# Kernel tuning notes

Measured on AMD Instinct MI355X. Metric: run time of the kernel, lower is better.

The kernel has to match this reference:

```python
import jax, jax.numpy as jnp
import numpy as np
from jax import lax

# ---- configuration (matches init_kwargs) ----
B, C_DATA, C_FEAT, H, W = 2, 8, 8, 160, 160
K = 7                      # number of soft nearest neighbors
PS, STRIDE, WIN = 10, 5, 15
FEAT, C_EMB = 64, 8
N1 = (H - PS) // STRIDE + 1   # 31, no padding needed
N2 = (W - PS) // STRIDE + 1   # 31
NEG_INF = -1e9


def _conv3(x, w, b):
    y = lax.conv_general_dilated(x, w, (1, 1), 'SAME',
                                 dimension_numbers=('NCHW', 'OIHW', 'NCHW'))
    return y + b[None, :, None, None]


def _cnn(x, w1, b1, w2, b2, w3, b3):
    # depth-3 DnCNN-style net: conv-relu-conv-relu-conv (bn=False, lastact=linear)
    h = jax.nn.relu(_conv3(x, w1, b1))
    h = jax.nn.relu(_conv3(h, w2, b2))
    return _conv3(h, w3, b3)


def _im2patch(x):
    # x: [b,c,H,W] -> [b,n1,n2,c*PS*PS]; patch flattened channel-major (c,p1,p2)
    ii = jnp.arange(N1)[:, None] * STRIDE + jnp.arange(PS)[None, :]  # [n1,PS]
    jj = jnp.arange(N2)[:, None] * STRIDE + jnp.arange(PS)[None, :]  # [n2,PS]
    p = x[:, :, ii[:, None, :, None], jj[None, :, None, :]]  # [b,c,n1,n2,PS,PS]
    p = jnp.transpose(p, (0, 2, 3, 1, 4, 5))
    return p.reshape(p.shape[0], N1, N2, -1)


def _n3block(x_data, x_faet, ew1, eb1, ew2, eb2, ew3, eb3,
             tw1, tb1, tw2, tb2, tw3, tb3):
    xe = _cnn(x_faet, ew1, eb1, ew2, eb2, ew3, eb3)      # [b,8,H,W] embeddings
    log_temp = _cnn(x_faet, tw1, tb1, tw2, tb2, tw3, tb3)  # [b,1,H,W]

    ye = _im2patch(xe)                        # [b,n1,n2,E]; queries == database
    yp = _im2patch(x_data)                    # [b,n1,n2,F]
    lt = _im2patch(log_temp).mean(-1)         # scalar log-temp per patch
    temp = jnp.exp(lt)[..., None]             # [b,n1,n2,1] (temp_bias = 1)

    S = min(WIN, N1, N2)
    R = S // 2
    base1 = jnp.clip(jnp.arange(N1) - R, 0, N1 - S)   # clamped window top-left
    base2 = jnp.clip(jnp.arange(N2) - R, 0, N2 - S)
    offs = jnp.stack(jnp.meshgrid(jnp.arange(S), jnp.arange(S), indexing='ij'),
                     axis=-1).reshape(-1, 2)          # [S*S,2]
    i1, i2 = jnp.arange(N1), jnp.arange(N2)
    yn = jnp.sum(ye * ye, axis=-1)            # [b,n1,n2] squared norms

    @jax.checkpoint
    def dist_step(carry, off):
        j1 = base1 + off[0]
        j2 = base2 + off[1]
        xs = ye[:, j1][:, :, j2]              # [b,n1,n2,E] candidate embedding
        xn = yn[:, j1][:, :, j2]
        dot = jnp.einsum('bije,bije->bij', ye, xs)
        d = yn + xn - 2.0 * dot               # squared euclidean distance
        self_m = (j1 == i1)[:, None] & (j2 == i2)[None, :]
        return carry, (d, self_m)

    _, (D, selfm) = lax.scan(dist_step, None, offs)
    D = jnp.moveaxis(D, 0, -1)                # [b,n1,n2,O], O=S*S
    selfm = jnp.moveaxis(selfm, 0, -1)        # [n1,n2,O]

    logits = -D / temp
    logits = jnp.where(selfm, NEG_INF, logits)   # exclude_self

    # continuous deterministic top-k (N3Net): w_j = softmax(a); a += log(1 - w_j)
    ws = []
    for _ in range(K):
        wgt = jax.nn.softmax(logits, axis=-1)
        ws.append(wgt)
        logits = logits + jnp.log1p(-jnp.minimum(wgt, 1.0 - 1e-6))
    Wk = jnp.stack(ws, axis=-1)               # [b,n1,n2,O,K]

    @jax.checkpoint
    def agg_step(z, args):
        off, wk = args                        # wk: [b,n1,n2,K]
        j1 = base1 + off[0]
        j2 = base2 + off[1]
        ys = yp[:, j1][:, :, j2]              # [b,n1,n2,F]
        return z + wk[..., :, None] * ys[..., None, :], None

    z0 = jnp.zeros(yp.shape[:3] + (K, yp.shape[-1]), yp.dtype)
    z, _ = lax.scan(agg_step, z0, (offs, jnp.moveaxis(Wk, 3, 0)))
    z = z - yp[..., None, :]                  # residue=True
    out_p = jnp.concatenate([yp[..., None, :], z], axis=3)  # [b,n1,n2,K+1,F]

    # fold patch volumes back to image, averaging overlaps
    b = out_p.shape[0]
    C = (K + 1) * C_DATA
    out_p = out_p.reshape(b, N1, N2, K + 1, C_DATA, PS, PS)
    out_p = jnp.transpose(out_p, (0, 3, 4, 1, 2, 5, 6)).reshape(b, C, N1, N2, PS, PS)
    rows = jnp.arange(N1)[:, None] * STRIDE + jnp.arange(PS)[None, :]
    cols = jnp.arange(N2)[:, None] * STRIDE + jnp.arange(PS)[None, :]
    lin = (rows[:, None, :, None] * W + cols[None, :, None, :]).reshape(-1)
    vals = out_p.reshape(b, C, -1)
    img = jnp.zeros((b, C, H * W), out_p.dtype).at[:, :, lin].add(vals)
    cnt = jnp.zeros((H * W,), out_p.dtype).at[lin].add(1.0)
    return (img / cnt).reshape(b, C, H, W)


def setup_inputs() -> dict:
    key = jax.random.key(0)
    ks = jax.random.split(key, 8)
    f32 = jnp.float32
    wn = lambda k, s: jax.random.normal(k, s, f32) * 0.05
    return dict(
        x_data=jax.random.normal(ks[0], (B, C_DATA, H, W), f32),
        x_faet=jax.random.normal(ks[1], (B, C_FEAT, H, W), f32),
        ew1=wn(ks[2], (FEAT, C_FEAT, 3, 3)), eb1=jnp.zeros((FEAT,), f32),
        ew2=wn(ks[3], (FEAT, FEAT, 3, 3)), eb2=jnp.zeros((FEAT,), f32),
        ew3=wn(ks[4], (C_EMB, FEAT, 3, 3)), eb3=jnp.zeros((C_EMB,), f32),
        tw1=wn(ks[5], (FEAT, C_FEAT, 3, 3)), tb1=jnp.zeros((FEAT,), f32),
        tw2=wn(ks[6], (FEAT, FEAT, 3, 3)), tb2=jnp.zeros((FEAT,), f32),
        tw3=wn(ks[7], (1, FEAT, 3, 3)), tb3=jnp.zeros((1,), f32),
    )


def reference(x_data, x_faet, ew1, eb1, ew2, eb2, ew3, eb3,
              tw1, tb1, tw2, tb2, tw3, tb3):
    return _n3block(x_data, x_faet, ew1, eb1, ew2, eb2, ew3, eb3,
                    tw1, tb1, tw2, tb2, tw3, tb3)
```

## Files before the change

kernel.cpp:

```cpp
#include <hip/hip_runtime.h>
#include <math.h>

#define BN 2
#define HH 160
#define WW 160
#define CDATA 8
#define PS 10
#define STR 5
#define N1 31
#define N2 31
#define NSITE (N1*N2)
#define SITES (BN*NSITE)
#define SWIN 15
#define NOFF 225
#define KK 7
#define EDIM 800
#define NPIX 25600
#define LP 40
#define KP 480
#define COLP 992
#define GP 34
#define KSPLIT 5

typedef __attribute__((ext_vector_type(8))) short s8v;
typedef __attribute__((ext_vector_type(8))) unsigned short u8v;
typedef __attribute__((ext_vector_type(4))) unsigned short u4v;
typedef __attribute__((ext_vector_type(4))) float f4v;

__device__ __forceinline__ unsigned short f2bf(float f) {
    unsigned u = __float_as_uint(f);
    return (unsigned short)((u + 0x7FFFu + ((u >> 16) & 1u)) >> 16);
}
__device__ __forceinline__ float bf2f(unsigned short h) {
    return __uint_as_float(((unsigned)h) << 16);
}

__global__ __launch_bounds__(256) void prep_k(const float* __restrict__ xd,
                                              const float* __restrict__ ew2,
                                              const float* __restrict__ tw2,
                                              const float* __restrict__ ew1,
                                              const float* __restrict__ tw1,
                                              const float* __restrict__ ew3,
                                              const float* __restrict__ tw3,
                                              unsigned short* __restrict__ ypT,
                                              unsigned short* __restrict__ wp,
                                              unsigned short* __restrict__ wp1,
                                              unsigned short* __restrict__ wp3) {
    int blk = blockIdx.x;
    int t = threadIdx.x;
    if (blk < 1600) {
        int b = blk / 800, e = blk % 800;
        int cd = e & 7, pp = e >> 3;
        int pi = pp / 10, pj = pp % 10;
        const float* src = xd + ((size_t)(b * 8 + cd) * HH + pi) * WW + pj;
        unsigned short* dst = ypT + (size_t)blk * COLP;
        for (int it = 0; it < 4; ++it) {
            int col = it * 256 + t;
            if (col < COLP) {
                int j1 = col >> 5, j2 = col & 31;
                unsigned short v = 0;
                if (j2 < 31) v = f2bf(src[(j1 * 5) * WW + j2 * 5]);
                dst[col] = v;
            }
        }
    } else if (blk < 1888) {
        int idx = (blk - 1600) * 256 + t;
        int which = idx / (64 * 576); int r = idx % (64 * 576);
        int n = r / 576, k = r % 576;
        int p = k / 64, c = k % 64;
        const float* w = which ? tw2 : ew2;
        wp[idx] = f2bf(w[(n * 64 + c) * 9 + p]);
    } else if (blk < 1936) {
        int idx = (blk - 1888) * 256 + t;
        if (idx < 128 * 96) {
            int n = idx / 96, k = idx % 96;
            int tap = k >> 3, c = k & 7;
            unsigned short v = 0;
            if (tap < 9) {
                const float* w = (n < 64) ? ew1 : tw1;
                v = f2bf(w[((n & 63) * 8 + c) * 9 + tap]);
            }
            wp1[idx] = v;
        }
    } else {
        int idx = (blk - 1936) * 256 + t;
        if (idx < 2 * 16 * 576) {
            int which = idx / (16 * 576); int r = idx % (16 * 576);
            int n = r / 576, k = r % 576;
            int tap = k / 64, c = k % 64;
            float w = 0.f; bool lo = false;
            if (which == 0) { w = ew3[((n & 7) * 64 + c) * 9 + tap]; lo = (n >= 8); }
            else if (n < 2) { w = tw3[c * 9 + tap]; lo = (n == 1); }
            unsigned short hi = f2bf(w);
            wp3[idx] = lo ? f2bf(w - bf2f(hi)) : hi;
            if (which == 1 && n >= 2) wp3[idx] = 0;
        }
    }
}

__global__ __launch_bounds__(256) void conv1_mfma_k(const float* __restrict__ xf,
                                                    const unsigned short* __restrict__ wp1,
                                                    const float* __restrict__ eb1,
                                                    const float* __restrict__ tb1,
                                                    unsigned short* __restrict__ h1) {
    __shared__ unsigned short Al[128 * LP];
    __shared__ unsigned short Bl[64 * LP];
    const int t = threadIdx.x;
    const int m0 = blockIdx.x * 64;
    const int wv = t >> 6, lane = t & 63;
    f4v acc[2][4];
    #pragma unroll
    for (int fj = 0; fj < 2; ++fj)
        #pragma unroll
        for (int fi = 0; fi < 4; ++fi) { f4v z = {0.f,0.f,0.f,0.f}; acc[fj][fi] = z; }
    const int mp = m0 + (t >> 2);
    const int b = mp / NPIX, rp = mp % NPIX;
    const int py = rp / WW, px = rp % WW;
    for (int ks = 0; ks < 3; ++ks) {
        int tap = ks * 4 + (t & 3);
        int dy = tap / 3 - 1, dx = tap % 3 - 1;
        int yy = py + dy, xx = px + dx;
        bool ok = (tap < 9) && yy >= 0 && yy < HH && xx >= 0 && xx < WW;
        u8v bv;
        #pragma unroll
        for (int c = 0; c < 8; ++c)
            bv[c] = ok ? f2bf(xf[((size_t)(b * 8 + c)) * NPIX + yy * WW + xx]) : 0;
        __syncthreads();
        *(u8v*)(Bl + (t >> 2) * LP + (t & 3) * 8) = bv;
        #pragma unroll
        for (int it = 0; it < 2; ++it) {
            int idx = t + it * 256;
            int row = idx >> 2, seg = idx & 3;
            *(u8v*)(Al + row * LP + seg * 8) = *(const u8v*)(wp1 + row * 96 + ks * 32 + seg * 8);
        }
        __syncthreads();
        s8v af[2], bf[4];
        #pragma unroll
        for (int fj = 0; fj < 2; ++fj)
            af[fj] = *(const s8v*)((const short*)Al + (wv * 32 + fj * 16 + (lane & 15)) * LP + (lane >> 4) * 8);
        #pragma unroll
        for (int fi = 0; fi < 4; ++fi)
            bf[fi] = *(const s8v*)((const short*)Bl + (fi * 16 + (lane & 15)) * LP + (lane >> 4) * 8);
        #pragma unroll
        for (int fj = 0; fj < 2; ++fj)
            #pragma unroll
            for (int fi = 0; fi < 4; ++fi)
                acc[fj][fi] = __builtin_amdgcn_mfma_f32_16x16x32_bf16(af[fj], bf[fi], acc[fj][fi], 0, 0, 0);
    }
    #pragma unroll
    for (int fj = 0; fj < 2; ++fj) {
        int nb = wv * 32 + fj * 16 + (lane >> 4) * 4;
        float bias4[4];
        #pragma unroll
        for (int c = 0; c < 4; ++c) {
            int n = nb + c;
            bias4[c] = (n < 64) ? eb1[n] : tb1[n - 64];
        }
        #pragma unroll
        for (int fi = 0; fi < 4; ++fi) {
            int mm = m0 + fi * 16 + (lane & 15);
            ushort4 o;
            o.x = f2bf(fmaxf(acc[fj][fi][0] + bias4[0], 0.f));
            o.y = f2bf(fmaxf(acc[fj][fi][1] + bias4[1], 0.f));
            o.z = f2bf(fmaxf(acc[fj][fi][2] + bias4[2], 0.f));
            o.w = f2bf(fmaxf(acc[fj][fi][3] + bias4[3], 0.f));
            *(ushort4*)(h1 + (size_t)mm * 128 + nb) = o;
        }
    }
}

__global__ __launch_bounds__(256) void conv2_mfma_k(const unsigned short* __restrict__ h1,
                                                    const unsigned short* __restrict__ wp,
                                                    const float* __restrict__ eb2,
                                                    const float* __restrict__ tb2,
                                                    unsigned short* __restrict__ h2) {
    __shared__ unsigned short Al[64 * LP];
    __shared__ unsigned short Bl[128 * LP];
    const int t = threadIdx.x;
    const int which = blockIdx.y;
    const int m0 = blockIdx.x * 128;
    const int wv = t >> 6, lane = t & 63;
    f4v acc[4][2];
    #pragma unroll
    for (int nf = 0; nf < 4; ++nf)
        #pragma unroll
        for (int mf = 0; mf < 2; ++mf) { f4v z = {0.f,0.f,0.f,0.f}; acc[nf][mf] = z; }
    const unsigned short* wb = wp + (size_t)which * 64 * 576;
    const int sm = t >> 2, sq = (t & 3) * 8;
    const int mp0 = m0 + sm;
    const int b0 = mp0 / NPIX, rp0 = mp0 % NPIX;
    const int py0 = rp0 / WW, px0 = rp0 % WW;
    const int mp1 = m0 + 64 + sm;
    const int b1_ = mp1 / NPIX, rp1 = mp1 % NPIX;
    const int py1 = rp1 / WW, px1 = rp1 % WW;
    for (int step = 0; step < 18; ++step) {
        const int p = step >> 1, ch = (step & 1) * 32;
        const int dy = p / 3 - 1, dx = p % 3 - 1;
        s8v av = *(const s8v*)(wb + sm * 576 + p * 64 + ch + sq);
        s8v bv0, bv1;
        #pragma unroll
        for (int j = 0; j < 8; j++) { bv0[j] = 0; bv1[j] = 0; }
        int yy = py0 + dy, xx = px0 + dx;
        if (yy >= 0 && yy < HH && xx >= 0 && xx < WW)
            bv0 = *(const s8v*)((const short*)h1 + ((size_t)b0 * NPIX + yy * WW + xx) * 128 + which * 64 + ch + sq);
        yy = py1 + dy; xx = px1 + dx;
        if (yy >= 0 && yy < HH && xx >= 0 && xx < WW)
            bv1 = *(const s8v*)((const short*)h1 + ((size_t)b1_ * NPIX + yy * WW + xx) * 128 + which * 64 + ch + sq);
        __syncthreads();
        *(s8v*)((short*)Al + sm * LP + sq) = av;
        *(s8v*)((short*)Bl + sm * LP + sq) = bv0;
        *(s8v*)((short*)Bl + (64 + sm) * LP + sq) = bv1;
        __syncthreads();
        s8v af[4], bf[2];
        #pragma unroll
        for (int nf = 0; nf < 4; ++nf)
            af[nf] = *(const s8v*)((const short*)Al + (nf * 16 + (lane & 15)) * LP + (lane >> 4) * 8);
        #pragma unroll
        for (int mf = 0; mf < 2; ++mf)
            bf[mf] = *(const s8v*)((const short*)Bl + (wv * 32 + mf * 16 + (lane & 15)) * LP + (lane >> 4) * 8);
        #pragma unroll
        for (int nf = 0; nf < 4; ++nf)
            #pragma unroll
            for (int mf = 0; mf < 2; ++mf)
                acc[nf][mf] = __builtin_amdgcn_mfma_f32_16x16x32_bf16(af[nf], bf[mf], acc[nf][mf], 0, 0, 0);
    }
    const float* bias = which ? tb2 : eb2;
    #pragma unroll
    for (int nf = 0; nf < 4; ++nf) {
        int nb = nf * 16 + (lane >> 4) * 4;
        f4v bv4 = *(const f4v*)(bias + nb);
        #pragma unroll
        for (int mf = 0; mf < 2; ++mf) {
            int mm = m0 + wv * 32 + mf * 16 + (lane & 15);
            ushort4 o;
            o.x = f2bf(fmaxf(acc[nf][mf][0] + bv4[0], 0.f));
            o.y = f2bf(fmaxf(acc[nf][mf][1] + bv4[1], 0.f));
            o.z = f2bf(fmaxf(acc[nf][mf][2] + bv4[2], 0.f));
            o.w = f2bf(fmaxf(acc[nf][mf][3] + bv4[3], 0.f));
            *(ushort4*)(h2 + ((size_t)which * 51200 + mm) * 64 + nb) = o;
        }
    }
}

__global__ __launch_bounds__(256) void conv3_mfma_k(const unsigned short* __restrict__ h2,
                                                    const unsigned short* __restrict__ wp3,
                                                    const float* __restrict__ eb3,
                                                    const float* __restrict__ tb3,
                                                    unsigned short* __restrict__ xeH,
                                                    unsigned short* __restrict__ xeL,
                                                    float* __restrict__ splane,
                                                    float* __restrict__ ltm) {
    __shared__ unsigned short Al[16 * LP];
    __shared__ unsigned short Bl[128 * LP];
    const int t = threadIdx.x;
    const int which = blockIdx.y;
    const int m0 = blockIdx.x * 128;
    const int wv = t >> 6, lane = t & 63;
    f4v acc[2];
    { f4v z = {0.f,0.f,0.f,0.f}; acc[0] = z; acc[1] = z; }
    const unsigned short* wb = wp3 + (size_t)which * 16 * 576;
    const int sm = t >> 2, sq = (t & 3) * 8;
    const int mp0 = m0 + sm;
    const int b0 = mp0 / NPIX, rp0 = mp0 % NPIX;
    const int py0 = rp0 / WW, px0 = rp0 % WW;
    const int mp1 = m0 + 64 + sm;
    const int b1_ = mp1 / NPIX, rp1 = mp1 % NPIX;
    const int py1 = rp1 / WW, px1 = rp1 % WW;
    for (int step = 0; step < 18; ++step) {
        const int p = step >> 1, ch = (step & 1) * 32;
        const int dy = p / 3 - 1, dx = p % 3 - 1;
        s8v av;
        if (t < 64) av = *(const s8v*)(wb + (t >> 2) * 576 + p * 64 + ch + (t & 3) * 8);
        s8v bv0, bv1;
        #pragma unroll
        for (int j = 0; j < 8; j++) { bv0[j] = 0; bv1[j] = 0; }
        int yy = py0 + dy, xx = px0 + dx;
        if (yy >= 0 && yy < HH && xx >= 0 && xx < WW)
            bv0 = *(const s8v*)((const short*)h2 + ((size_t)which * 51200 + (size_t)b0 * NPIX + yy * WW + xx) * 64 + ch + sq);
        yy = py1 + dy; xx = px1 + dx;
        if (yy >= 0 && yy < HH && xx >= 0 && xx < WW)
            bv1 = *(const s8v*)((const short*)h2 + ((size_t)which * 51200 + (size_t)b1_ * NPIX + yy * WW + xx) * 64 + ch + sq);
        __syncthreads();
        if (t < 64) *(s8v*)((short*)Al + (t >> 2) * LP + (t & 3) * 8) = av;
        *(s8v*)((short*)Bl + sm * LP + sq) = bv0;
        *(s8v*)((short*)Bl + (64 + sm) * LP + sq) = bv1;
        __syncthreads();
        s8v af = *(const s8v*)((const short*)Al + (lane & 15) * LP + (lane >> 4) * 8);
        #pragma unroll
        for (int mf = 0; mf < 2; ++mf) {
            s8v bf = *(const s8v*)((const short*)Bl + (wv * 32 + mf * 16 + (lane & 15)) * LP + (lane >> 4) * 8);
            acc[mf] = __builtin_amdgcn_mfma_f32_16x16x32_bf16(af, bf, acc[mf], 0, 0, 0);
        }
    }
    #pragma unroll
    for (int mf = 0; mf < 2; ++mf) {
        int mm = m0 + wv * 32 + mf * 16 + (lane & 15);
        if (which == 0) {
            f4v hilo;
            #pragma unroll
            for (int c = 0; c < 4; ++c)
                hilo[c] = acc[mf][c] + __shfl_xor(acc[mf][c], 32);
            if (lane < 32) {
                int nb = (lane >> 4) * 4;
                u4v hs, ls;
                float ss = 0.f;
                #pragma unroll
                for (int c = 0; c < 4; ++c) {
                    float v = hilo[c] + eb3[nb + c];
                    unsigned short h = f2bf(v);
                    hs[c] = h;
                    ls[c] = f2bf(v - bf2f(h));
                    ss += v * v;
                }
                *(u4v*)(xeH + (size_t)mm * 8 + nb) = hs;
                *(u4v*)(xeL + (size_t)mm * 8 + nb) = ls;
                ss += __shfl_xor(ss, 16);
                if (lane < 16) splane[mm] = ss;
            }
        } else {
            if ((lane >> 4) == 0)
                ltm[mm] = acc[mf][0] + acc[mf][1] + tb3[0];
        }
    }
}

__global__ __launch_bounds__(256) void ynt_k(const float* __restrict__ splane,
                                             const float* __restrict__ ltm,
                                             float* __restrict__ yn,
                                             float* __restrict__ tempv) {
    int wv = threadIdx.x >> 6, lane = threadIdx.x & 63;
    int wid = blockIdx.x * 4 + wv;
    if (wid >= SITES) return;
    int b = wid / NSITE; int ij = wid % NSITE;
    int i1 = ij / N2, i2 = ij % N2;
    float s1 = 0.f, s2 = 0.f;
    for (int p = lane; p < 100; p += 64) {
        int rr = p / 10, q = p % 10;
        int idx = b * NPIX + (i1 * STR + rr) * WW + i2 * STR + q;
        s1 += splane[idx];
        s2 += ltm[idx];
    }
    #pragma unroll
    for (int o = 32; o; o >>= 1) { s1 += __shfl_xor(s1, o); s2 += __shfl_xor(s2, o); }
    if (lane == 0) {
        yn[wid] = s1;
        tempv[wid] = expf(s2 * (1.f / 100.f));
    }
}

__global__ __launch_bounds__(256) void gram_mfma_k(const unsigned short* __restrict__ xeH,
                                                   const unsigned short* __restrict__ xeL,
                                                   float* __restrict__ dotsC) {
    __shared__ unsigned short AsH[32 * GP], AsL[32 * GP];
    __shared__ unsigned short BsH[256 * GP], BsL[256 * GP];
    int blk = blockIdx.x;
    int kc = blk % KSPLIT; int r = blk / KSPLIT;
    int nh = r & 1; r >>= 1;
    int b = r / N1, i1 = r % N1;
    int b1 = min(max(i1 - 7, 0), 16);
    int t = threadIdx.x;
    int wv = t >> 6, lane = t & 63;
    f4v acc[2][4];
    #pragma unroll
    for (int mt = 0; mt < 2; ++mt)
        #pragma unroll
        for (int nt = 0; nt < 4; ++nt) { f4v z = {0.f,0.f,0.f,0.f}; acc[mt][nt] = z; }
    const size_t pbase = (size_t)b * NPIX;
    for (int ks = kc * 5; ks < kc * 5 + 5; ++ks) {
        __syncthreads();
        {
            int idx = t & 127;
            int row = idx >> 2, seg = idx & 3;
            int p = ks * 4 + seg;
            int rr = p / 10, q = p - rr * 10;
            u8v v;
            #pragma unroll
            for (int u = 0; u < 8; ++u) v[u] = 0;
            if (row < 31) {
                size_t a = (pbase + (size_t)(i1 * STR + rr) * WW + row * STR + q) * 8;
                v = *(const u8v*)((t < 128 ? xeH : xeL) + a);
            }
            *(u8v*)((t < 128 ? AsH : AsL) + row * GP + seg * 8) = v;
        }
        #pragma unroll
        for (int rep = 0; rep < 8; ++rep) {
            int idx = t + rep * 256;
            int isH = idx < 1024;
            int id2 = idx & 1023;
            int row = id2 >> 2, seg = id2 & 3;
            int dj = nh * 8 + (row >> 5), j2 = row & 31;
            int p = ks * 4 + seg;
            int rr = p / 10, q = p - rr * 10;
            u8v v;
            #pragma unroll
            for (int u = 0; u < 8; ++u) v[u] = 0;
            if (dj < 15 && j2 < 31) {
                size_t a = (pbase + (size_t)((b1 + dj) * STR + rr) * WW + j2 * STR + q) * 8;
                v = *(const u8v*)((isH ? xeH : xeL) + a);
            }
            *(u8v*)((isH ? BsH : BsL) + row * GP + seg * 8) = v;
        }
        __syncthreads();
        s8v afH[2], afL[2], bfH[4], bfL[4];
        #pragma unroll
        for (int mt = 0; mt < 2; ++mt) {
            int ar = mt * 16 + (lane & 15);
            afH[mt] = *(const s8v*)((const short*)AsH + ar * GP + (lane >> 4) * 8);
            afL[mt] = *(const s8v*)((const short*)AsL + ar * GP + (lane >> 4) * 8);
        }
        #pragma unroll
        for (int nt = 0; nt < 4; ++nt) {
            int br = wv * 64 + nt * 16 + (lane & 15);
            bfH[nt] = *(const s8v*)((const short*)BsH + br * GP + (lane >> 4) * 8);
            bfL[nt] = *(const s8v*)((const short*)BsL + br * GP + (lane >> 4) * 8);
        }
        #pragma unroll
        for (int mt = 0; mt < 2; ++mt)
            #pragma unroll
            for (int nt = 0; nt < 4; ++nt) {
                acc[mt][nt] = __builtin_amdgcn_mfma_f32_16x16x32_bf16(afH[mt], bfH[nt], acc[mt][nt], 0, 0, 0);
                acc[mt][nt] = __builtin_amdgcn_mfma_f32_16x16x32_bf16(afH[mt], bfL[nt], acc[mt][nt], 0, 0, 0);
                acc[mt][nt] = __builtin_amdgcn_mfma_f32_16x16x32_bf16(afL[mt], bfH[nt], acc[mt][nt], 0, 0, 0);
            }
    }
    float* dk = dotsC + (size_t)kc * SITES * NOFF;
    #pragma unroll
    for (int mt = 0; mt < 2; ++mt) {
        int i2b = mt * 16 + (lane >> 4) * 4;
        #pragma unroll
        for (int nt = 0; nt < 4; ++nt) {
            int n = wv * 64 + nt * 16 + (lane & 15);
            int dj = nh * 8 + (n >> 5), j2 = n & 31;
            if (dj >= 15 || j2 >= 31) continue;
            #pragma unroll
            for (int c = 0; c < 4; ++c) {
                int i2 = i2b + c;
                if (i2 >= 31) continue;
                int b2 = min(max(i2 - 7, 0), 16);
                int dc = j2 - b2;
                if (dc < 0 || dc >= SWIN) continue;
                size_t site = (size_t)((b * N1 + i1) * N2 + i2);
                dk[site * NOFF + dj * SWIN + dc] = acc[mt][nt][c];
            }
        }
    }
}

__global__ __launch_bounds__(256) void softmax_awrite_k(const float* __restrict__ dotsC,
                                                        const float* __restrict__ yn,
                                                        const float* __restrict__ tempv,
                                                        unsigned short* __restrict__ Aglob) {
    __shared__ float sw[4][228];
    int wv = threadIdx.x >> 6, lane = threadIdx.x & 63;
    int wid = blockIdx.x * 4 + wv;
    bool active = (wid < SITES);
    int wids = active ? wid : (SITES - 1);
    int b = wids / NSITE; int ij = wids % NSITE;
    int i1 = ij / N2, i2 = ij % N2;
    int b1 = min(max(i1 - 7, 0), 16);
    int b2 = min(max(i2 - 7, 0), 16);
    int pglob = i2 >> 1, s = i2 & 1;
    unsigned short* Abase = Aglob + (size_t)((b * N1 + i1) * 256) * KP;
    float yns = yn[wids];
    float tvi = 1.f / tempv[wids];
    float lg[4];
    #pragma unroll
    for (int r = 0; r < 4; ++r) {
        int t = lane + 64 * r;
        lg[r] = -1e9f;
        if (t < NOFF) {
            float dot = 0.f;
            #pragma unroll
            for (int kc = 0; kc < KSPLIT; ++kc)
                dot += dotsC[((size_t)kc * SITES + wids) * NOFF + t];
            int dj = t / SWIN, dc = t % SWIN;
            int j1 = b1 + dj, j2 = b2 + dc;
            float xn = yn[(b * N1 + j1) * N2 + j2];
            float d = yns + xn - 2.f * dot;
            lg[r] = -d * tvi;
            if (j1 == i1 && j2 == i2) lg[r] = -1e9f;
        }
    }
    for (int k = 0; k < KK; ++k) {
        float m = fmaxf(fmaxf(lg[0], lg[1]), fmaxf(lg[2], lg[3]));
        #pragma unroll
        for (int o = 32; o; o >>= 1) m = fmaxf(m, __shfl_xor(m, o));
        float ex[4]; float ssum = 0.f;
        #pragma unroll
        for (int r = 0; r < 4; ++r) { ex[r] = __expf(lg[r] - m); ssum += ex[r]; }
        #pragma unroll
        for (int o = 32; o; o >>= 1) ssum += __shfl_xor(ssum, o);
        float inv = 1.f / ssum;
        #pragma unroll
        for (int r = 0; r < 4; ++r) {
            float wgt = ex[r] * inv;
            int t = lane + 64 * r;
            if (t < NOFF) sw[wv][t] = wgt;
            lg[r] += log1pf(-fminf(wgt, 1.f - 1e-6f));
        }
        __syncthreads();
        if (active && lane < 60) {
            u8v o;
            #pragma unroll
            for (int u = 0; u < 8; ++u) {
                int n = lane * 8 + u;
                int dj = n >> 5, j2 = n & 31;
                int dc = j2 - b2;
                o[u] = (j2 < 31 && dc >= 0 && dc < SWIN) ? f2bf(sw[wv][dj * SWIN + dc]) : (unsigned short)0;
            }
            int m_ = 16 * pglob + k + 7 * s;
            *(u8v*)(Abase + (size_t)m_ * KP + lane * 8) = o;
        }
        __syncthreads();
    }
    if (active && s == 0 && lane < 60) {
        u8v z;
        #pragma unroll
        for (int u = 0; u < 8; ++u) z[u] = 0;
        *(u8v*)(Abase + (size_t)(16 * pglob + 14) * KP + lane * 8) = z;
        *(u8v*)(Abase + (size_t)(16 * pglob + 15) * KP + lane * 8) = z;
        if (i2 == 30) {
            #pragma unroll
            for (int sl = 7; sl < 14; ++sl)
                *(u8v*)(Abase + (size_t)(16 * 15 + sl) * KP + lane * 8) = z;
        }
    }
}

__global__ __launch_bounds__(256) void agg_gemm_k(const unsigned short* __restrict__ Aglob,
                                                  const unsigned short* __restrict__ ypT,
                                                  unsigned short* __restrict__ zbuf) {
    __shared__ unsigned short As[128 * 40];
    __shared__ unsigned short Bs[160 * 40];
    int blk = blockIdx.x;
    int b = blk / 310; int r = blk % 310;
    int i1 = r / 10; int r2 = r % 10;
    int mh = r2 / 5, nc = r2 % 5;
    int b1 = min(max(i1 - 7, 0), 16);
    int t = threadIdx.x;
    int wv = t >> 6, lane = t & 63;
    int wm = (wv & 1) * 64, we = (wv >> 1) * 80;
    const unsigned short* Ab = Aglob + ((size_t)(b * N1 + i1) * 256 + mh * 128) * KP;
    const unsigned short* Bb = ypT + ((size_t)b * 800 + nc * 160) * COLP + b1 * 32;
    f4v accr[4][5];
    #pragma unroll
    for (int mt = 0; mt < 4; ++mt)
        #pragma unroll
        for (int et = 0; et < 5; ++et) { f4v z = {0.f,0.f,0.f,0.f}; accr[mt][et] = z; }
    for (int ks = 0; ks < 15; ++ks) {
        __syncthreads();
        #pragma unroll
        for (int it = 0; it < 2; ++it) {
            int idx = t + it * 256;
            int row = idx >> 2, seg = idx & 3;
            *(u8v*)(As + row * 40 + seg * 8) = *(const u8v*)(Ab + (size_t)row * KP + ks * 32 + seg * 8);
        }
        #pragma unroll
        for (int it = 0; it < 3; ++it) {
            int idx = t + it * 256;
            if (idx < 640) {
                int row = idx >> 2, seg = idx & 3;
                *(u8v*)(Bs + row * 40 + seg * 8) = *(const u8v*)(Bb + (size_t)row * COLP + ks * 32 + seg * 8);
            }
        }
        __syncthreads();
        s8v af[4], bf[5];
        #pragma unroll
        for (int mt = 0; mt < 4; ++mt)
            af[mt] = *(const s8v*)((const short*)As + (wm + mt * 16 + (lane & 15)) * 40 + (lane >> 4) * 8);
        #pragma unroll
        for (int et = 0; et < 5; ++et)
            bf[et] = *(const s8v*)((const short*)Bs + (we + et * 16 + (lane & 15)) * 40 + (lane >> 4) * 8);
        #pragma unroll
        for (int mt = 0; mt < 4; ++mt)
            #pragma unroll
            for (int et = 0; et < 5; ++et)
                accr[mt][et] = __builtin_amdgcn_mfma_f32_16x16x32_bf16(af[mt], bf[et], accr[mt][et], 0, 0, 0);
    }
    unsigned short* zb = zbuf + ((size_t)(b * N1 + i1) * 256 + mh * 128) * 800 + nc * 160;
    #pragma unroll
    for (int mt = 0; mt < 4; ++mt) {
        int mrow = wm + mt * 16 + (lane >> 4) * 4;
        #pragma unroll
        for (int et = 0; et < 5; ++et) {
            int ecol = we + et * 16 + (lane & 15);
            #pragma unroll
            for (int c = 0; c < 4; ++c)
                zb[(size_t)(mrow + c) * 800 + ecol] = f2bf(accr[mt][et][c]);
        }
    }
}

__global__ __launch_bounds__(256) void finalize_k(const unsigned short* __restrict__ zbuf,
                                                  const float* __restrict__ xd,
                                                  float* __restrict__ out) {
    int pid = blockIdx.x * 256 + threadIdx.x;
    if (pid >= BN * NPIX) return;
    int b = pid / NPIX, pix = pid % NPIX;
    int h = pix / WW, w_ = pix % WW;
    int lo1 = max(0, (h - 5) / 5),  hi1 = min(30, h / 5);
    int lo2 = max(0, (w_ - 5) / 5), hi2 = min(30, w_ / 5);
    float cntinv = 1.f / (float)((hi1 - lo1 + 1) * (hi2 - lo2 + 1));
    float xv[8];
    #pragma unroll
    for (int cd = 0; cd < 8; ++cd) {
        xv[cd] = xd[((size_t)(b * 8 + cd)) * NPIX + pix];
        out[((size_t)(b * 64 + cd)) * NPIX + pix] = xv[cd];
    }
    for (int k = 0; k < KK; ++k) {
        float s[8];
        #pragma unroll
        for (int cd = 0; cd < 8; ++cd) s[cd] = 0.f;
        for (int i1 = lo1; i1 <= hi1; ++i1) {
            int pi = h - 5 * i1;
            for (int i2 = lo2; i2 <= hi2; ++i2) {
                int pj = w_ - 5 * i2;
                int m = 16 * (i2 >> 1) + k + 7 * (i2 & 1);
                const unsigned short* zp = zbuf + ((size_t)(b * N1 + i1) * 256 + m) * 800 + (pi * 10 + pj) * 8;
                u8v zv = *(const u8v*)zp;
                #pragma unroll
                for (int cd = 0; cd < 8; ++cd) s[cd] += bf2f(zv[cd]);
            }
        }
        #pragma unroll
        for (int cd = 0; cd < 8; ++cd)
            out[((size_t)(b * 64 + (k + 1) * 8 + cd)) * NPIX + pix] = s[cd] * cntinv - xv[cd];
    }
}

extern "C" void kernel_launch(void* const* d_in, const int* in_sizes, int n_in,
                              void* d_out, int out_size, void* d_ws, size_t ws_size,
                              hipStream_t stream) {
    (void)in_sizes; (void)n_in; (void)out_size; (void)ws_size;
    const float* x_data = (const float*)d_in[0];
    const float* x_faet = (const float*)d_in[1];
    const float* ew1 = (const float*)d_in[2];  const float* eb1 = (const float*)d_in[3];
    const float* ew2 = (const float*)d_in[4];  const float* eb2 = (const float*)d_in[5];
    const float* ew3 = (const float*)d_in[6];  const float* eb3 = (const float*)d_in[7];
    const float* tw1 = (const float*)d_in[8];  const float* tb1 = (const float*)d_in[9];
    const float* tw2 = (const float*)d_in[10]; const float* tb2 = (const float*)d_in[11];
    const float* tw3 = (const float*)d_in[12]; const float* tb3 = (const float*)d_in[13];
    float* out = (float*)d_out;

    char* base = (char*)d_ws;
    unsigned short* h1 = (unsigned short*)(base);
    unsigned short* h2 = (unsigned short*)(base + 13107200);
    unsigned short* wp1 = (unsigned short*)(base + 13107200);
    unsigned short* wp = (unsigned short*)(base + 26214400);
    float* yn    = (float*)(base + 26361856);
    float* tempv = (float*)(base + 26370048);
    unsigned short* ypT = (unsigned short*)(base + 26378240);
    unsigned short* xeH = (unsigned short*)(base + 29552640);
    unsigned short* xeL = (unsigned short*)(base + 30371840);
    float* ltm    = (float*)(base + 31191040);
    float* splane = (float*)(base + 31395840);
    unsigned short* wp3 = (unsigned short*)(base + 37546240);
    unsigned short* Aglob = (unsigned short*)(base + 29552640);
    float* dotsC = (float*)h2;
    unsigned short* zbuf = (unsigned short*)base;

    prep_k<<<2008, 256, 0, stream>>>(x_data, ew2, tw2, ew1, tw1, ew3, tw3, ypT, wp, wp1, wp3);
    conv1_mfma_k<<<800, 256, 0, stream>>>(x_faet, wp1, eb1, tb1, h1);
    conv2_mfma_k<<<dim3(400, 2), 256, 0, stream>>>(h1, wp, eb2, tb2, h2);
    conv3_mfma_k<<<dim3(400, 2), 256, 0, stream>>>(h2, wp3, eb3, tb3, xeH, xeL, splane, ltm);

    ynt_k<<<(SITES + 3) / 4, 256, 0, stream>>>(splane, ltm, yn, tempv);
    gram_mfma_k<<<BN * N1 * 2 * KSPLIT, 256, 0, stream>>>(xeH, xeL, dotsC);
    softmax_awrite_k<<<(SITES + 3) / 4, 256, 0, stream>>>(dotsC, yn, tempv, Aglob);

    agg_gemm_k<<<BN * 310, 256, 0, stream>>>(Aglob, ypT, zbuf);
    finalize_k<<<(BN * NPIX + 255) / 256, 256, 0, stream>>>(zbuf, x_data, out);
}
```

Before: 165.0 us.

## Merge independent kernels into shared launches and widen conv2 K-step per barrier

Moves the ypT patch transpose out of the weight-prep kernel into extra blocks of the conv1 launch, and folds the yn/temperature reduction kernel into the gram kernel as extra blocks, removing one kernel launch and letting independent work overlap. Conv2 now stages 64 channels per tap into shared memory (padded stride 72) and issues two MFMA k-steps per pair of barriers, halving the number of synchronisations. This doubles conv2 shared memory per block, which may reduce occupancy.

```diff
diff --git a/kernel.cpp b/kernel.cpp
--- a/kernel.cpp
+++ b/kernel.cpp
@@ -17,10 +17,13 @@
 #define EDIM 800
 #define NPIX 25600
 #define LP 40
+#define LP2 72
 #define KP 480
 #define COLP 992
 #define GP 34
 #define KSPLIT 5
+#define GRAMBLKS (BN*N1*2*KSPLIT)
+#define YNTBLKS ((SITES+3)/4)
 
 typedef __attribute__((ext_vector_type(8))) short s8v;
 typedef __attribute__((ext_vector_type(8))) unsigned short u8v;
@@ -35,43 +38,26 @@
     return __uint_as_float(((unsigned)h) << 16);
 }
 
-__global__ __launch_bounds__(256) void prep_k(const float* __restrict__ xd,
-                                              const float* __restrict__ ew2,
+__global__ __launch_bounds__(256) void prep_k(const float* __restrict__ ew2,
                                               const float* __restrict__ tw2,
                                               const float* __restrict__ ew1,
                                               const float* __restrict__ tw1,
                                               const float* __restrict__ ew3,
                                               const float* __restrict__ tw3,
-                                              unsigned short* __restrict__ ypT,
                                               unsigned short* __restrict__ wp,
                                               unsigned short* __restrict__ wp1,
                                               unsigned short* __restrict__ wp3) {
     int blk = blockIdx.x;
     int t = threadIdx.x;
-    if (blk < 1600) {
-        int b = blk / 800, e = blk % 800;
-        int cd = e & 7, pp = e >> 3;
-        int pi = pp / 10, pj = pp % 10;
-        const float* src = xd + ((size_t)(b * 8 + cd) * HH + pi) * WW + pj;
-        unsigned short* dst = ypT + (size_t)blk * COLP;
-        for (int it = 0; it < 4; ++it) {
-            int col = it * 256 + t;
-            if (col < COLP) {
-                int j1 = col >> 5, j2 = col & 31;
-                unsigned short v = 0;
-                if (j2 < 31) v = f2bf(src[(j1 * 5) * WW + j2 * 5]);
-                dst[col] = v;
-            }
-        }
-    } else if (blk < 1888) {
-        int idx = (blk - 1600) * 256 + t;
+    if (blk < 288) {
+        int idx = blk * 256 + t;
         int which = idx / (64 * 576); int r = idx % (64 * 576);
         int n = r / 576, k = r % 576;
         int p = k / 64, c = k % 64;
         const float* w = which ? tw2 : ew2;
         wp[idx] = f2bf(w[(n * 64 + c) * 9 + p]);
-    } else if (blk < 1936) {
-        int idx = (blk - 1888) * 256 + t;
+    } else if (blk < 336) {
+        int idx = (blk - 288) * 256 + t;
         if (idx < 128 * 96) {
             int n = idx / 96, k = idx % 96;
             int tap = k >> 3, c = k & 7;
@@ -83,7 +69,7 @@
             wp1[idx] = v;
         }
     } else {
-        int idx = (blk - 1936) * 256 + t;
+        int idx = (blk - 336) * 256 + t;
         if (idx < 2 * 16 * 576) {
             int which = idx / (16 * 576); int r = idx % (16 * 576);
             int n = r / 576, k = r % 576;
@@ -98,14 +84,34 @@
     }
 }
 
-__global__ __launch_bounds__(256) void conv1_mfma_k(const float* __restrict__ xf,
-                                                    const unsigned short* __restrict__ wp1,
-                                                    const float* __restrict__ eb1,
-                                                    const float* __restrict__ tb1,
-                                                    unsigned short* __restrict__ h1) {
+__global__ __launch_bounds__(256) void conv1_ypt_k(const float* __restrict__ xf,
+                                                   const float* __restrict__ xd,
+                                                   const unsigned short* __restrict__ wp1,
+                                                   const float* __restrict__ eb1,
+                                                   const float* __restrict__ tb1,
+                                                   unsigned short* __restrict__ h1,
+                                                   unsigned short* __restrict__ ypT) {
+    const int t = threadIdx.x;
+    if (blockIdx.x >= 800) {
+        int row = blockIdx.x - 800;
+        int b = row / 800, e = row % 800;
+        int cd = e & 7, pp = e >> 3;
+        int pi = pp / 10, pj = pp % 10;
+        const float* src = xd + ((size_t)(b * 8 + cd) * HH + pi) * WW + pj;
+        unsigned short* dst = ypT + (size_t)row * COLP;
+        for (int it = 0; it < 4; ++it) {
+            int col = it * 256 + t;
+            if (col < COLP) {
+                int j1 = col >> 5, j2 = col & 31;
+                unsigned short v = 0;
+                if (j2 < 31) v = f2bf(src[(j1 * 5) * WW + j2 * 5]);
+                dst[col] = v;
+            }
+        }
+        return;
+    }
     __shared__ unsigned short Al[128 * LP];
     __shared__ unsigned short Bl[64 * LP];
-    const int t = threadIdx.x;
     const int m0 = blockIdx.x * 64;
     const int wv = t >> 6, lane = t & 63;
     f4v acc[2][4];
@@ -174,8 +180,8 @@
                                                     const float* __restrict__ eb2,
                                                     const float* __restrict__ tb2,
                                                     unsigned short* __restrict__ h2) {
-    __shared__ unsigned short Al[64 * LP];
-    __shared__ unsigned short Bl[128 * LP];
+    __shared__ unsigned short Al[64 * LP2];
+    __shared__ unsigned short Bl[128 * LP2];
     const int t = threadIdx.x;
     const int which = blockIdx.y;
     const int m0 = blockIdx.x * 128;
@@ -193,36 +199,48 @@
     const int mp1 = m0 + 64 + sm;
     const int b1_ = mp1 / NPIX, rp1 = mp1 % NPIX;
     const int py1 = rp1 / WW, px1 = rp1 % WW;
-    for (int step = 0; step < 18; ++step) {
-        const int p = step >> 1, ch = (step & 1) * 32;
+    for (int p = 0; p < 9; ++p) {
         const int dy = p / 3 - 1, dx = p % 3 - 1;
-        s8v av = *(const s8v*)(wb + sm * 576 + p * 64 + ch + sq);
-        s8v bv0, bv1;
-        #pragma unroll
-        for (int j = 0; j < 8; j++) { bv0[j] = 0; bv1[j] = 0; }
+        s8v av[2], bv0[2], bv1[2];
+        #pragma unroll
+        for (int hh = 0; hh < 2; ++hh) {
+            av[hh] = *(const s8v*)(wb + sm * 576 + p * 64 + hh * 32 + sq);
+            #pragma unroll
+            for (int j = 0; j < 8; j++) { bv0[hh][j] = 0; bv1[hh][j] = 0; }
+        }
         int yy = py0 + dy, xx = px0 + dx;
-        if (yy >= 0 && yy < HH && xx >= 0 && xx < WW)
-            bv0 = *(const s8v*)((const short*)h1 + ((size_t)b0 * NPIX + yy * WW + xx) * 128 + which * 64 + ch + sq);
+        if (yy >= 0 && yy < HH && xx >= 0 && xx < WW) {
+            const short* src = (const short*)h1 + ((size_t)b0 * NPIX + yy * WW + xx) * 128 + which * 64 + sq;
+            bv0[0] = *(const s8v*)src; bv0[1] = *(const s8v*)(src + 32);
+        }
         yy = py1 + dy; xx = px1 + dx;
-        if (yy >= 0 && yy < HH && xx >= 0 && xx < WW)
-            bv1 = *(const s8v*)((const short*)h1 + ((size_t)b1_ * NPIX + yy * WW + xx) * 128 + which * 64 + ch + sq);
-        __syncthreads();
-        *(s8v*)((short*)Al + sm * LP + sq) = av;
-        *(s8v*)((short*)Bl + sm * LP + sq) = bv0;
-        *(s8v*)((short*)Bl + (64 + sm) * LP + sq) = bv1;
-        __syncthreads();
-        s8v af[4], bf[2];
-        #pragma unroll
-        for (int nf = 0; nf < 4; ++nf)
-            af[nf] = *(const s8v*)((const short*)Al + (nf * 16 + (lane & 15)) * LP + (lane >> 4) * 8);
-        #pragma unroll
-        for (int mf = 0; mf < 2; ++mf)
-            bf[mf] = *(const s8v*)((const short*)Bl + (wv * 32 + mf * 16 + (lane & 15)) * LP + (lane >> 4) * 8);
-        #pragma unroll
-        for (int nf = 0; nf < 4; ++nf)
+        if (yy >= 0 && yy < HH && xx >= 0 && xx < WW) {
+            const short* src = (const short*)h1 + ((size_t)b1_ * NPIX + yy * WW + xx) * 128 + which * 64 + sq;
+            bv1[0] = *(const s8v*)src; bv1[1] = *(const s8v*)(src + 32);
+        }
+        __syncthreads();
+        #pragma unroll
+        for (int hh = 0; hh < 2; ++hh) {
+            *(s8v*)((short*)Al + sm * LP2 + hh * 32 + sq) = av[hh];
+            *(s8v*)((short*)Bl + sm * LP2 + hh * 32 + sq) = bv0[hh];
+            *(s8v*)((short*)Bl + (64 + sm) * LP2 + hh * 32 + sq) = bv1[hh];
+        }
+        __syncthreads();
+        #pragma unroll
+        for (int kk = 0; kk < 2; ++kk) {
+            s8v af[4], bf[2];
+            #pragma unroll
+            for (int nf = 0; nf < 4; ++nf)
+                af[nf] = *(const s8v*)((const short*)Al + (nf * 16 + (lane & 15)) * LP2 + kk * 32 + (lane >> 4) * 8);
             #pragma unroll
             for (int mf = 0; mf < 2; ++mf)
-                acc[nf][mf] = __builtin_amdgcn_mfma_f32_16x16x32_bf16(af[nf], bf[mf], acc[nf][mf], 0, 0, 0);
+                bf[mf] = *(const s8v*)((const short*)Bl + (wv * 32 + mf * 16 + (lane & 15)) * LP2 + kk * 32 + (lane >> 4) * 8);
+            #pragma unroll
+            for (int nf = 0; nf < 4; ++nf)
+                #pragma unroll
+                for (int mf = 0; mf < 2; ++mf)
+                    acc[nf][mf] = __builtin_amdgcn_mfma_f32_16x16x32_bf16(af[nf], bf[mf], acc[nf][mf], 0, 0, 0);
+        }
     }
     const float* bias = which ? tb2 : eb2;
     #pragma unroll
@@ -324,33 +342,34 @@
     }
 }
 
-__global__ __launch_bounds__(256) void ynt_k(const float* __restrict__ splane,
-                                             const float* __restrict__ ltm,
-                                             float* __restrict__ yn,
-                                             float* __restrict__ tempv) {
-    int wv = threadIdx.x >> 6, lane = threadIdx.x & 63;
-    int wid = blockIdx.x * 4 + wv;
-    if (wid >= SITES) return;
-    int b = wid / NSITE; int ij = wid % NSITE;
-    int i1 = ij / N2, i2 = ij % N2;
-    float s1 = 0.f, s2 = 0.f;
-    for (int p = lane; p < 100; p += 64) {
-        int rr = p / 10, q = p % 10;
-        int idx = b * NPIX + (i1 * STR + rr) * WW + i2 * STR + q;
-        s1 += splane[idx];
-        s2 += ltm[idx];
-    }
-    #pragma unroll
-    for (int o = 32; o; o >>= 1) { s1 += __shfl_xor(s1, o); s2 += __shfl_xor(s2, o); }
-    if (lane == 0) {
-        yn[wid] = s1;
-        tempv[wid] = expf(s2 * (1.f / 100.f));
-    }
-}
-
-__global__ __launch_bounds__(256) void gram_mfma_k(const unsigned short* __restrict__ xeH,
-                                                   const unsigned short* __restrict__ xeL,
-                                                   float* __restrict__ dotsC) {
+__global__ __launch_bounds__(256) void gram_ynt_k(const unsigned short* __restrict__ xeH,
+                                                  const unsigned short* __restrict__ xeL,
+                                                  const float* __restrict__ splane,
+                                                  const float* __restrict__ ltm,
+                                                  float* __restrict__ dotsC,
+                                                  float* __restrict__ yn,
+                                                  float* __restrict__ tempv) {
+    if (blockIdx.x >= GRAMBLKS) {
+        int wv = threadIdx.x >> 6, lane = threadIdx.x & 63;
+        int wid = (blockIdx.x - GRAMBLKS) * 4 + wv;
+        if (wid >= SITES) return;
+        int b = wid / NSITE; int ij = wid % NSITE;
+        int i1 = ij / N2, i2 = ij % N2;
+        float s1 = 0.f, s2 = 0.f;
+        for (int p = lane; p < 100; p += 64) {
+            int rr = p / 10, q = p % 10;
+            int idx = b * NPIX + (i1 * STR + rr) * WW + i2 * STR + q;
+            s1 += splane[idx];
+            s2 += ltm[idx];
+        }
+        #pragma unroll
+        for (int o = 32; o; o >>= 1) { s1 += __shfl_xor(s1, o); s2 += __shfl_xor(s2, o); }
+        if (lane == 0) {
+            yn[wid] = s1;
+            tempv[wid] = expf(s2 * (1.f / 100.f));
+        }
+        return;
+    }
     __shared__ unsigned short AsH[32 * GP], AsL[32 * GP];
     __shared__ unsigned short BsH[256 * GP], BsL[256 * GP];
     int blk = blockIdx.x;
@@ -659,14 +678,13 @@
     float* dotsC = (float*)h2;
     unsigned short* zbuf = (unsigned short*)base;
 
-    prep_k<<<2008, 256, 0, stream>>>(x_data, ew2, tw2, ew1, tw1, ew3, tw3, ypT, wp, wp1, wp3);
-    conv1_mfma_k<<<800, 256, 0, stream>>>(x_faet, wp1, eb1, tb1, h1);
+    prep_k<<<408, 256, 0, stream>>>(ew2, tw2, ew1, tw1, ew3, tw3, wp, wp1, wp3);
+    conv1_ypt_k<<<800 + 1600, 256, 0, stream>>>(x_faet, x_data, wp1, eb1, tb1, h1, ypT);
     conv2_mfma_k<<<dim3(400, 2), 256, 0, stream>>>(h1, wp, eb2, tb2, h2);
     conv3_mfma_k<<<dim3(400, 2), 256, 0, stream>>>(h2, wp3, eb3, tb3, xeH, xeL, splane, ltm);
 
-    ynt_k<<<(SITES + 3) / 4, 256, 0, stream>>>(splane, ltm, yn, tempv);
-    gram_mfma_k<<<BN * N1 * 2 * KSPLIT, 256, 0, stream>>>(xeH, xeL, dotsC);
-    softmax_awrite_k<<<(SITES + 3) / 4, 256, 0, stream>>>(dotsC, yn, tempv, Aglob);
+    gram_ynt_k<<<GRAMBLKS + YNTBLKS, 256, 0, stream>>>(xeH, xeL, splane, ltm, dotsC, yn, tempv);
+    softmax_awrite_k<<<YNTBLKS, 256, 0, stream>>>(dotsC, yn, tempv, Aglob);
 
     agg_gemm_k<<<BN * 310, 256, 0, stream>>>(Aglob, ypT, zbuf);
     finalize_k<<<(BN * NPIX + 255) / 256, 256, 0, stream>>>(zbuf, x_data, out);
```

Result: faster. 159.1 us, median of 5 (-3.6%).
